# Kernel optimization log

Measured on AMD Instinct MI355X. Metric: run time of the kernel, lower is better.

The kernel has to match this reference:

```python
import jax, jax.numpy as jnp
import numpy as np

N_NODES = 100000
N_EDGES = 1600000
IN_DIM, HID_DIM, OUT_DIM = 128, 128, 64


def setup_inputs() -> dict:
    key = jax.random.key(0)
    ks = jax.random.split(key, 5)
    x = jax.random.normal(ks[0], (N_NODES, IN_DIM), dtype=jnp.float32)
    edge_index = jax.random.randint(ks[1], (2, N_EDGES), 0, N_NODES, dtype=jnp.int64)
    W1 = jax.random.normal(ks[2], (IN_DIM, HID_DIM), dtype=jnp.float32) * (1.0 / np.sqrt(IN_DIM))
    b1 = jnp.zeros((HID_DIM,), dtype=jnp.float32)
    W2 = jax.random.normal(ks[3], (HID_DIM, OUT_DIM), dtype=jnp.float32) * (1.0 / np.sqrt(HID_DIM))
    b2 = jnp.zeros((OUT_DIM,), dtype=jnp.float32)
    return {"x": x, "edge_index": edge_index, "W1": W1, "b1": b1, "W2": W2, "b2": b2}


def _gcn_conv(h, row, col, norm, b, n_nodes):
    # h: [N, F] already linearly transformed; message = norm_e * h[src]; scatter-add to dst
    msg = h[row] * norm[:, None]                      # [E+N, F]
    out = jax.ops.segment_sum(msg, col, num_segments=n_nodes)
    return out + b


def reference(x, edge_index, W1, b1, W2, b2):
    n = x.shape[0]
    loops = jnp.arange(n, dtype=edge_index.dtype)
    row = jnp.concatenate([edge_index[0], loops])     # sources (incl. self loops)
    col = jnp.concatenate([edge_index[1], loops])     # targets
    # symmetric normalization: deg over targets with unit edge weights
    deg = jax.ops.segment_sum(jnp.ones_like(col, dtype=x.dtype), col, num_segments=n)
    dinv = jnp.where(deg > 0, jax.lax.rsqrt(jnp.maximum(deg, 1.0)), 0.0)
    norm = dinv[row] * dinv[col]                      # [E+N]
    h = jax.nn.relu(_gcn_conv(x @ W1, row, col, norm, b1, n))
    out = _gcn_conv(h @ W2, row, col, norm, b2, n)
    return out.mean(axis=0)                           # [OUT_DIM]
```

## Files before the change

### kernel.cpp

```cpp
#include <hip/hip_runtime.h>

#define N_NODES 100000
#define N_EDGES 1600000
#define IN_DIM 128
#define HID_DIM 128
#define OUT_DIM 64
#define BKT_SHIFT 7
#define BKT_SIZE 128
#define NBKT ((N_NODES + BKT_SIZE - 1) / BKT_SIZE)
#define B1 256
#define HIST_N (NBKT * B1)
#define HIST_N2 (2 * HIST_N)
#define GEMM_BLKS ((N_NODES + 127) / 128)

typedef float v2f __attribute__((ext_vector_type(2)));
typedef float v4f __attribute__((ext_vector_type(4)));
typedef short v8s __attribute__((ext_vector_type(8)));

__device__ __forceinline__ int permb(int b) { return ((b & 7) << 5) | (b >> 3); }

__device__ __forceinline__ unsigned int f2bf(float f) {
  unsigned int u = __float_as_uint(f);
  return (u + 0x7FFFu + ((u >> 16) & 1u)) >> 16;
}

template <bool HI>
__device__ __forceinline__ v2f cvt8(unsigned int u) {
  return __builtin_amdgcn_cvt_pk_f32_fp8((int)u, HI);
}

__device__ __forceinline__ float wdec(unsigned int p) {
  return __uint_as_float((p >> 17) << 16);
}

__device__ __forceinline__ void load4(const void* ei, int is64, int half, int base,
                                      int* v) {
  if (is64) {
    const long long* e = (const long long*)ei + (size_t)half * N_EDGES + base;
    longlong2 a = *(const longlong2*)e;
    longlong2 b = *(const longlong2*)(e + 2);
    v[0] = (int)a.x; v[1] = (int)a.y; v[2] = (int)b.x; v[3] = (int)b.y;
  } else {
    const int* e = (const int*)ei + (size_t)half * N_EDGES + base;
    int4 a = *(const int4*)e;
    v[0] = a.x; v[1] = a.y; v[2] = a.z; v[3] = a.w;
  }
}

__device__ __forceinline__ int detect64_block(const unsigned int* ei, int* sh) {
  if (threadIdx.x == 0) *sh = 0;
  __syncthreads();
  if (ei[1 + 2 * threadIdx.x] != 0u) *sh = 1;
  __syncthreads();
  return (*sh == 0) ? 1 : 0;
}

__global__ __launch_bounds__(256) void front_kernel(const float* __restrict__ x,
                                                    const float* __restrict__ W,
                                                    const void* ei,
                                                    unsigned int* __restrict__ G,
                                                    int* hist, float* S) {
  __shared__ __align__(16) char smem[2 * 128 * 136 * 2];
  if (blockIdx.x >= GEMM_BLKS) {
    int* hd = (int*)smem;
    int* hs = hd + NBKT;
    int* sh = hs + NBKT;
    const int hb = blockIdx.x - GEMM_BLKS;
    const int pj = permb(hb);
    if (hb == 0 && threadIdx.x < HID_DIM) S[threadIdx.x] = 0.f;
    const int is64 = detect64_block((const unsigned int*)ei, sh);
    for (int k = threadIdx.x; k < NBKT; k += 256) { hd[k] = 0; hs[k] = 0; }
    __syncthreads();
    for (int g = hb * 256 + threadIdx.x; g < N_EDGES / 4; g += B1 * 256) {
      int r[4], c[4];
      load4(ei, is64, 0, g * 4, r);
      load4(ei, is64, 1, g * 4, c);
#pragma unroll
      for (int k = 0; k < 4; k++) {
        atomicAdd(&hd[c[k] >> BKT_SHIFT], 1);
        atomicAdd(&hs[r[k] >> BKT_SHIFT], 1);
      }
    }
    __syncthreads();
    for (int k = threadIdx.x; k < NBKT; k += 256) {
      hist[k * B1 + pj] = hd[k];
      hist[HIST_N + k * B1 + pj] = hs[k];
    }
    return;
  }
  typedef unsigned short us_row[136];
  us_row* lx = (us_row*)smem;
  us_row* lwt = (us_row*)(smem + 128 * 136 * 2);
  const int t = threadIdx.x;
  const int row0 = blockIdx.x * 128;

  {
    const float4* W4 = (const float4*)W;
    for (int it = 0; it < 16; ++it) {
      int idx = t + 256 * it;
      int k = idx >> 5, c4 = (idx & 31) * 4;
      float4 w = W4[idx];
      lwt[c4 + 0][k] = (unsigned short)f2bf(w.x);
      lwt[c4 + 1][k] = (unsigned short)f2bf(w.y);
      lwt[c4 + 2][k] = (unsigned short)f2bf(w.z);
      lwt[c4 + 3][k] = (unsigned short)f2bf(w.w);
    }
  }
  {
    const float4* x4 = (const float4*)(x + (size_t)row0 * IN_DIM);
    for (int it = 0; it < 16; ++it) {
      int idx = t + 256 * it;
      int r = idx >> 5, kq = (idx & 31) * 4;
      float4 v = make_float4(0.f, 0.f, 0.f, 0.f);
      if (row0 + r < N_NODES) v = x4[idx];
      unsigned int p0 = (f2bf(v.y) << 16) | f2bf(v.x);
      unsigned int p1 = (f2bf(v.w) << 16) | f2bf(v.z);
      *(uint2*)&lx[r][kq] = make_uint2(p0, p1);
    }
  }
  __syncthreads();

  const int lane = t & 63;
  const int wv = t >> 6;
  const int m0 = wv * 32;
  const int lrow = lane & 15;
  const int lk = (lane >> 4) * 8;

  v4f acc[2][8];
#pragma unroll
  for (int si = 0; si < 2; si++)
#pragma unroll
    for (int n = 0; n < 8; n++) acc[si][n] = (v4f){0.f, 0.f, 0.f, 0.f};

#pragma unroll
  for (int kk = 0; kk < 128; kk += 32) {
    v8s a0 = *(const v8s*)&lx[m0 + lrow][kk + lk];
    v8s a1 = *(const v8s*)&lx[m0 + 16 + lrow][kk + lk];
#pragma unroll
    for (int n = 0; n < 8; n++) {
      v8s b = *(const v8s*)&lwt[n * 16 + lrow][kk + lk];
      acc[0][n] = __builtin_amdgcn_mfma_f32_16x16x32_bf16(a0, b, acc[0][n], 0, 0, 0);
      acc[1][n] = __builtin_amdgcn_mfma_f32_16x16x32_bf16(a1, b, acc[1][n], 0, 0, 0);
    }
  }

  unsigned char* G8 = (unsigned char*)G;
#pragma unroll
  for (int si = 0; si < 2; si++)
#pragma unroll
    for (int n = 0; n < 8; n++) {
      int colg = n * 16 + (lane & 15);
#pragma unroll
      for (int i = 0; i < 4; i++) {
        int r = row0 + m0 + si * 16 + (lane >> 4) * 4 + i;
        if (r < N_NODES) {
          float v = acc[si][n][i];
          int pk = __builtin_amdgcn_cvt_pk_fp8_f32(v, v, 0, false);
          G8[(size_t)r * HID_DIM + colg] = (unsigned char)(pk & 0xFF);
        }
      }
    }
}

__global__ void scan1_kernel(int* arr, int* bsum, int n) {
  __shared__ int tmp[256];
  int i = blockIdx.x * 256 + threadIdx.x;
  int v = (i < n) ? arr[i] : 0;
  tmp[threadIdx.x] = v;
  __syncthreads();
  for (int off = 1; off < 256; off <<= 1) {
    int t2 = (threadIdx.x >= off) ? tmp[threadIdx.x - off] : 0;
    __syncthreads();
    tmp[threadIdx.x] += t2;
    __syncthreads();
  }
  if (i < n) arr[i] = tmp[threadIdx.x] - v;
  if (threadIdx.x == 255) bsum[blockIdx.x] = tmp[255];
}

__global__ void scan2_kernel(int* bsum, int nb) {
  __shared__ int tmp[1024];
  const int t = threadIdx.x;
  int v0 = (2 * t < nb) ? bsum[2 * t] : 0;
  int v1 = (2 * t + 1 < nb) ? bsum[2 * t + 1] : 0;
  int s = v0 + v1;
  tmp[t] = s;
  __syncthreads();
  for (int off = 1; off < 1024; off <<= 1) {
    int t2 = (t >= off) ? tmp[t - off] : 0;
    __syncthreads();
    tmp[t] += t2;
    __syncthreads();
  }
  int excl = tmp[t] - s;
  if (2 * t < nb) bsum[2 * t] = excl;
  if (2 * t + 1 < nb) bsum[2 * t + 1] = excl + v0;
}

__global__ __launch_bounds__(256) void scatter_kernel(const void* ei, const int* hist,
                                                      const int* bsum,
                                                      unsigned int* pairs) {
  __shared__ int cd[NBKT], cs[NBKT], sh[1];
  const int is64 = detect64_block((const unsigned int*)ei, sh);
  const int pj = permb(blockIdx.x);
  for (int k = threadIdx.x; k < NBKT; k += 256) {
    cd[k] = hist[k * B1 + pj] + bsum[k];
    cs[k] = hist[HIST_N + k * B1 + pj] + bsum[NBKT + k];
  }
  __syncthreads();
  for (int g = blockIdx.x * 256 + threadIdx.x; g < N_EDGES / 4; g += B1 * 256) {
    int r[4], c[4];
    load4(ei, is64, 0, g * 4, r);
    load4(ei, is64, 1, g * 4, c);
#pragma unroll
    for (int k = 0; k < 4; k++) {
      int pd = atomicAdd(&cd[c[k] >> BKT_SHIFT], 1);
      pairs[pd] = ((unsigned int)(c[k] & (BKT_SIZE - 1)) << 17) | (unsigned int)r[k];
      int ps = atomicAdd(&cs[r[k] >> BKT_SHIFT], 1);
      pairs[ps] = ((unsigned int)(r[k] & (BKT_SIZE - 1)) << 17) | (unsigned int)c[k];
    }
  }
}

__global__ __launch_bounds__(256) void csrA_kernel(const int* hist, const int* bsum,
                                                   const unsigned int* pairs,
                                                   int* rowptr, float* dinv) {
  __shared__ int cnt[BKT_SIZE], sc[BKT_SIZE];
  const int k = blockIdx.x;
  const int base = hist[k * B1] + bsum[k];
  const int end = (k == NBKT - 1) ? N_EDGES : hist[(k + 1) * B1] + bsum[k + 1];
  const int nseg = end - base;
  const int l = threadIdx.x;
  if (l < BKT_SIZE) cnt[l] = 0;
  __syncthreads();
  for (int i = l; i < nseg; i += 256) atomicAdd(&cnt[pairs[base + i] >> 17], 1);
  __syncthreads();
  if (l < BKT_SIZE) sc[l] = cnt[l];
  __syncthreads();
  for (int off = 1; off < BKT_SIZE; off <<= 1) {
    int v = (l < BKT_SIZE && l >= off) ? sc[l - off] : 0;
    __syncthreads();
    if (l < BKT_SIZE) sc[l] += v;
    __syncthreads();
  }
  if (l < BKT_SIZE) {
    int excl = sc[l] - cnt[l];
    int v = k * BKT_SIZE + l;
    if (v < N_NODES) {
      rowptr[v] = base + excl;
      dinv[v] = rsqrtf((float)(cnt[l] + 1));
    }
  }
  if (k == NBKT - 1 && l == 0) rowptr[N_NODES] = N_EDGES;
}

__global__ __launch_bounds__(256) void csrBout_kernel(const int* hist, const int* bsum,
                                                      const unsigned int* pairs,
                                                      const int* __restrict__ rowptr,
                                                      const float* __restrict__ dinv,
                                                      unsigned int* __restrict__ csr,
                                                      float* __restrict__ wacc) {
  if (blockIdx.x < NBKT) {
    __shared__ int cur[BKT_SIZE];
    const int k = blockIdx.x;
    const int base = hist[k * B1] + bsum[k];
    const int end = (k == NBKT - 1) ? N_EDGES : hist[(k + 1) * B1] + bsum[k + 1];
    const int nseg = end - base;
    const int l = threadIdx.x;
    if (l < BKT_SIZE) {
      int v = k * BKT_SIZE + l;
      cur[l] = (v < N_NODES) ? rowptr[v] : 0;
    }
    __syncthreads();
    for (int i = l; i < nseg; i += 256) {
      unsigned int pk = pairs[base + i];
      unsigned int src = pk & 0x1FFFFu;
      int pos = atomicAdd(&cur[pk >> 17], 1);
      unsigned int bits = f2bf(dinv[src]);
      csr[pos] = (bits << 17) | src;
    }
    return;
  }
  __shared__ float fb[BKT_SIZE];
  const int k = blockIdx.x - NBKT;
  const int base = hist[HIST_N + k * B1] + bsum[NBKT + k];
  const int end =
      (k == NBKT - 1) ? 2 * N_EDGES : hist[HIST_N + (k + 1) * B1] + bsum[NBKT + k + 1];
  if (threadIdx.x < BKT_SIZE) fb[threadIdx.x] = 0.f;
  __syncthreads();
  for (int i = base + threadIdx.x; i < end; i += 256) {
    unsigned int pk = pairs[i];
    atomicAdd(&fb[pk >> 17], dinv[pk & 0x1FFFFu]);
  }
  __syncthreads();
  int v = k * BKT_SIZE + threadIdx.x;
  if (threadIdx.x < BKT_SIZE && v < N_NODES) wacc[v] = fb[threadIdx.x];
}

__global__ __launch_bounds__(256) void aggregate_kernel(
    const unsigned int* __restrict__ G, const int* __restrict__ rowptr,
    const unsigned int* __restrict__ csr, const float* __restrict__ dinv,
    const float* __restrict__ wacc, const float* __restrict__ b1,
    float* __restrict__ S) {
  const int lane = threadIdx.x & 63;
  const int sub = lane & 31;
  const int half = lane >> 5;
  const int wid = blockIdx.x * 4 + (threadIdx.x >> 6);
  const int nwaves = gridDim.x * 4;
  const float4 b = ((const float4*)b1)[sub];
  v2f s01 = {0.f, 0.f}, s23 = {0.f, 0.f};

  for (int c = wid; c < N_NODES; c += nwaves) {
    const int start = rowptr[c];
    const int cnum = rowptr[c + 1] - start;
    const float d = dinv[c];
    v2f a01 = {0.f, 0.f}, a23 = {0.f, 0.f};
    if (half == 0) {
      unsigned int g = G[c * 32 + sub];
      a01 = cvt8<false>(g) * d;
      a23 = cvt8<true>(g) * d;
    }
    for (int j0 = 0; j0 < cnum; j0 += 64) {
      unsigned int pkl = 0;
      if (j0 + lane < cnum)
        pkl = __builtin_nontemporal_load(&csr[start + j0 + lane]);
      const int m = min(64, cnum - j0);
      int i = 0;
      for (; i + 8 <= m; i += 8) {
        unsigned int p0 = __shfl(pkl, i + half);
        unsigned int p1 = __shfl(pkl, i + 2 + half);
        unsigned int p2 = __shfl(pkl, i + 4 + half);
        unsigned int p3 = __shfl(pkl, i + 6 + half);
        unsigned int g0 = G[(p0 & 0x1FFFFu) * 32 + sub];
        unsigned int g1 = G[(p1 & 0x1FFFFu) * 32 + sub];
        unsigned int g2 = G[(p2 & 0x1FFFFu) * 32 + sub];
        unsigned int g3 = G[(p3 & 0x1FFFFu) * 32 + sub];
        float w0 = wdec(p0), w1 = wdec(p1), w2 = wdec(p2), w3 = wdec(p3);
        a01 += cvt8<false>(g0) * w0; a23 += cvt8<true>(g0) * w0;
        a01 += cvt8<false>(g1) * w1; a23 += cvt8<true>(g1) * w1;
        a01 += cvt8<false>(g2) * w2; a23 += cvt8<true>(g2) * w2;
        a01 += cvt8<false>(g3) * w3; a23 += cvt8<true>(g3) * w3;
      }
      for (; i + 2 <= m; i += 2) {
        unsigned int p = __shfl(pkl, i + half);
        unsigned int g = G[(p & 0x1FFFFu) * 32 + sub];
        float w = wdec(p);
        a01 += cvt8<false>(g) * w;
        a23 += cvt8<true>(g) * w;
      }
      if (i < m) {
        unsigned int p = __shfl(pkl, i);
        if (half == 0) {
          unsigned int g = G[(p & 0x1FFFFu) * 32 + sub];
          float w = wdec(p);
          a01 += cvt8<false>(g) * w;
          a23 += cvt8<true>(g) * w;
        }
      }
    }
    a01.x += __shfl(a01.x, sub + 32);
    a01.y += __shfl(a01.y, sub + 32);
    a23.x += __shfl(a23.x, sub + 32);
    a23.y += __shfl(a23.y, sub + 32);
    if (half == 0) {
      float wc = d * (wacc[c] + d);
      s01.x += wc * fmaxf(fmaf(d, a01.x, b.x), 0.f);
      s01.y += wc * fmaxf(fmaf(d, a01.y, b.y), 0.f);
      s23.x += wc * fmaxf(fmaf(d, a23.x, b.z), 0.f);
      s23.y += wc * fmaxf(fmaf(d, a23.y, b.w), 0.f);
    }
  }

  __shared__ float ls[HID_DIM];
  if (threadIdx.x < HID_DIM) ls[threadIdx.x] = 0.f;
  __syncthreads();
  if (half == 0) {
    atomicAdd(&ls[4 * sub + 0], s01.x);
    atomicAdd(&ls[4 * sub + 1], s01.y);
    atomicAdd(&ls[4 * sub + 2], s23.x);
    atomicAdd(&ls[4 * sub + 3], s23.y);
  }
  __syncthreads();
  if (threadIdx.x < HID_DIM) atomicAdd(&S[threadIdx.x], ls[threadIdx.x]);
}

__global__ void finish_kernel(const float* __restrict__ S, const float* __restrict__ W2,
                              const float* __restrict__ b2, float* __restrict__ out) {
  int j = threadIdx.x;
  float acc = 0.f;
  for (int k = 0; k < HID_DIM; k++) acc += S[k] * W2[k * OUT_DIM + j];
  out[j] = acc * (1.0f / N_NODES) + b2[j];
}

extern "C" void kernel_launch(void* const* d_in, const int* in_sizes, int n_in,
                              void* d_out, int out_size, void* d_ws, size_t ws_size,
                              hipStream_t stream) {
  const float* x  = (const float*)d_in[0];
  const void*  ei = d_in[1];
  const float* W1 = (const float*)d_in[2];
  const float* b1 = (const float*)d_in[3];
  const float* W2 = (const float*)d_in[4];
  const float* b2 = (const float*)d_in[5];
  float* out = (float*)d_out;

  char* p = (char*)d_ws;
  size_t off = 0;
  auto alloc = [&](size_t bytes) -> void* {
    void* r = p + off;
    off = (off + bytes + 63) & ~(size_t)63;
    return r;
  };
  int*   hist   = (int*)alloc((size_t)HIST_N2 * 4);
  int*   bsum   = (int*)alloc(2048 * 4);
  unsigned int* pairs = (unsigned int*)alloc((size_t)2 * N_EDGES * 4);
  int*   rowptr = (int*)alloc(((size_t)N_NODES + 1) * 4);
  unsigned int* csr = (unsigned int*)alloc((size_t)N_EDGES * 4);
  float* dinv   = (float*)alloc((size_t)N_NODES * 4);
  float* wacc   = (float*)alloc((size_t)N_NODES * 4);
  float* S      = (float*)alloc(HID_DIM * 4);
  unsigned int* G = (unsigned int*)alloc((size_t)N_NODES * HID_DIM);
  (void)ws_size; (void)n_in; (void)in_sizes; (void)out_size;

  const int NBH = HIST_N2 / 256;

  front_kernel<<<GEMM_BLKS + B1, 256, 0, stream>>>(x, W1, ei, G, hist, S);
  scan1_kernel<<<NBH, 256, 0, stream>>>(hist, bsum, HIST_N2);
  scan2_kernel<<<1, 1024, 0, stream>>>(bsum, NBH);
  scatter_kernel<<<B1, 256, 0, stream>>>(ei, hist, bsum, pairs);
  csrA_kernel<<<NBKT, 256, 0, stream>>>(hist, bsum, pairs, rowptr, dinv);
  csrBout_kernel<<<2 * NBKT, 256, 0, stream>>>(hist, bsum, pairs, rowptr, dinv, csr,
                                               wacc);
  aggregate_kernel<<<2048, 256, 0, stream>>>(G, rowptr, csr, dinv, wacc, b1, S);
  finish_kernel<<<1, 64, 0, stream>>>(S, W2, b2, out);
}
```

Measured before the change: 272.7 us.

## Restructure aggregation: quarter-wave edges, contiguous node chunks, prefetched CSR

The aggregation kernel now splits each wave into four 16-lane groups. Each lane gathers 8 bytes (uint2) of the fp8 feature row, so a wave processes four edges per gather step instead of two. Each wave takes a contiguous chunk of 13 nodes, loads their rowptr, dinv and wacc values once into lanes, and prefetches the next node's CSR entries while the current node is being processed. The changes aim to raise memory-level parallelism and cut per-node scalar loads. The cost is more register pressure, a two-step xor-shuffle reduction per node, and a masked tail path. Grid size with NPW=13 gives 8192 waves covering 106496 nodes, so all nodes are covered.

```diff
diff --git a/kernel.cpp b/kernel.cpp
--- a/kernel.cpp
+++ b/kernel.cpp
@@ -12,6 +12,8 @@
 #define HIST_N (NBKT * B1)
 #define HIST_N2 (2 * HIST_N)
 #define GEMM_BLKS ((N_NODES + 127) / 128)
+#define AGG_BLKS 2048
+#define NPW 13
 
 typedef float v2f __attribute__((ext_vector_type(2)));
 typedef float v4f __attribute__((ext_vector_type(4)));
@@ -31,6 +33,12 @@
 
 __device__ __forceinline__ float wdec(unsigned int p) {
   return __uint_as_float((p >> 17) << 16);
+}
+
+__device__ __forceinline__ float redq(float v) {
+  v += __shfl_xor(v, 16);
+  v += __shfl_xor(v, 32);
+  return v;
 }
 
 __device__ __forceinline__ void load4(const void* ei, int is64, int half, int base,
@@ -303,82 +311,122 @@
     const float* __restrict__ wacc, const float* __restrict__ b1,
     float* __restrict__ S) {
   const int lane = threadIdx.x & 63;
-  const int sub = lane & 31;
-  const int half = lane >> 5;
+  const int q = lane >> 4;
+  const int r = lane & 15;
   const int wid = blockIdx.x * 4 + (threadIdx.x >> 6);
-  const int nwaves = gridDim.x * 4;
-  const float4 b = ((const float4*)b1)[sub];
-  v2f s01 = {0.f, 0.f}, s23 = {0.f, 0.f};
-
-  for (int c = wid; c < N_NODES; c += nwaves) {
-    const int start = rowptr[c];
-    const int cnum = rowptr[c + 1] - start;
-    const float d = dinv[c];
-    v2f a01 = {0.f, 0.f}, a23 = {0.f, 0.f};
-    if (half == 0) {
-      unsigned int g = G[c * 32 + sub];
-      a01 = cvt8<false>(g) * d;
-      a23 = cvt8<true>(g) * d;
-    }
+  const int c0 = wid * NPW;
+  const uint2* __restrict__ G2 = (const uint2*)G;
+
+  int rp = 0;
+  float dvv = 0.f, wvv = 0.f;
+  {
+    const int ci = c0 + lane;
+    if (lane <= NPW && ci <= N_NODES) rp = rowptr[ci];
+    if (lane < NPW && ci < N_NODES) { dvv = dinv[ci]; wvv = wacc[ci]; }
+  }
+  const float4 bA = ((const float4*)b1)[2 * r];
+  const float4 bB = ((const float4*)b1)[2 * r + 1];
+
+  v2f s01 = {0.f, 0.f}, s23 = {0.f, 0.f}, s45 = {0.f, 0.f}, s67 = {0.f, 0.f};
+
+  const int nn = (c0 < N_NODES) ? min(NPW, N_NODES - c0) : 0;
+
+  int sNxt = __shfl(rp, 0);
+  int eNxt = __shfl(rp, 1);
+  unsigned int pwNxt = 0;
+  if (nn > 0 && sNxt + lane < eNxt)
+    pwNxt = __builtin_nontemporal_load(&csr[sNxt + lane]);
+
+  for (int k = 0; k < nn; ++k) {
+    const int sc = sNxt;
+    const int cnum = eNxt - sNxt;
+    unsigned int pw = pwNxt;
+    const float d = __shfl(dvv, k);
+    const float wa = __shfl(wvv, k);
+    if (k + 1 < nn) {
+      sNxt = __shfl(rp, k + 1);
+      eNxt = __shfl(rp, k + 2);
+      pwNxt = 0;
+      if (sNxt + lane < eNxt)
+        pwNxt = __builtin_nontemporal_load(&csr[sNxt + lane]);
+    }
+
+    v2f a01 = {0.f, 0.f}, a23 = {0.f, 0.f}, a45 = {0.f, 0.f}, a67 = {0.f, 0.f};
+    if (q == 0) {
+      uint2 g = G2[(size_t)(c0 + k) * 16 + r];
+      a01 += cvt8<false>(g.x) * d; a23 += cvt8<true>(g.x) * d;
+      a45 += cvt8<false>(g.y) * d; a67 += cvt8<true>(g.y) * d;
+    }
+
     for (int j0 = 0; j0 < cnum; j0 += 64) {
-      unsigned int pkl = 0;
-      if (j0 + lane < cnum)
-        pkl = __builtin_nontemporal_load(&csr[start + j0 + lane]);
+      if (j0 > 0) {
+        pw = 0;
+        if (j0 + lane < cnum)
+          pw = __builtin_nontemporal_load(&csr[sc + j0 + lane]);
+      }
       const int m = min(64, cnum - j0);
       int i = 0;
-      for (; i + 8 <= m; i += 8) {
-        unsigned int p0 = __shfl(pkl, i + half);
-        unsigned int p1 = __shfl(pkl, i + 2 + half);
-        unsigned int p2 = __shfl(pkl, i + 4 + half);
-        unsigned int p3 = __shfl(pkl, i + 6 + half);
-        unsigned int g0 = G[(p0 & 0x1FFFFu) * 32 + sub];
-        unsigned int g1 = G[(p1 & 0x1FFFFu) * 32 + sub];
-        unsigned int g2 = G[(p2 & 0x1FFFFu) * 32 + sub];
-        unsigned int g3 = G[(p3 & 0x1FFFFu) * 32 + sub];
-        float w0 = wdec(p0), w1 = wdec(p1), w2 = wdec(p2), w3 = wdec(p3);
-        a01 += cvt8<false>(g0) * w0; a23 += cvt8<true>(g0) * w0;
-        a01 += cvt8<false>(g1) * w1; a23 += cvt8<true>(g1) * w1;
-        a01 += cvt8<false>(g2) * w2; a23 += cvt8<true>(g2) * w2;
-        a01 += cvt8<false>(g3) * w3; a23 += cvt8<true>(g3) * w3;
-      }
-      for (; i + 2 <= m; i += 2) {
-        unsigned int p = __shfl(pkl, i + half);
-        unsigned int g = G[(p & 0x1FFFFu) * 32 + sub];
-        float w = wdec(p);
-        a01 += cvt8<false>(g) * w;
-        a23 += cvt8<true>(g) * w;
+      for (; i + 16 <= m; i += 16) {
+        float w[4];
+        uint2 g[4];
+#pragma unroll
+        for (int t = 0; t < 4; ++t) {
+          unsigned int p = __shfl(pw, i + 4 * t + q);
+          w[t] = wdec(p);
+          g[t] = G2[(size_t)(p & 0x1FFFFu) * 16 + r];
+        }
+#pragma unroll
+        for (int t = 0; t < 4; ++t) {
+          a01 += cvt8<false>(g[t].x) * w[t]; a23 += cvt8<true>(g[t].x) * w[t];
+          a45 += cvt8<false>(g[t].y) * w[t]; a67 += cvt8<true>(g[t].y) * w[t];
+        }
       }
       if (i < m) {
-        unsigned int p = __shfl(pkl, i);
-        if (half == 0) {
-          unsigned int g = G[(p & 0x1FFFFu) * 32 + sub];
-          float w = wdec(p);
-          a01 += cvt8<false>(g) * w;
-          a23 += cvt8<true>(g) * w;
+        float w[4];
+        uint2 g[4];
+#pragma unroll
+        for (int t = 0; t < 4; ++t) {
+          const int e = i + 4 * t + q;
+          unsigned int p = __shfl(pw, e & 63);
+          const bool vld = e < m;
+          w[t] = vld ? wdec(p) : 0.f;
+          g[t] = make_uint2(0u, 0u);
+          if (vld) g[t] = G2[(size_t)(p & 0x1FFFFu) * 16 + r];
+        }
+#pragma unroll
+        for (int t = 0; t < 4; ++t) {
+          a01 += cvt8<false>(g[t].x) * w[t]; a23 += cvt8<true>(g[t].x) * w[t];
+          a45 += cvt8<false>(g[t].y) * w[t]; a67 += cvt8<true>(g[t].y) * w[t];
         }
       }
     }
-    a01.x += __shfl(a01.x, sub + 32);
-    a01.y += __shfl(a01.y, sub + 32);
-    a23.x += __shfl(a23.x, sub + 32);
-    a23.y += __shfl(a23.y, sub + 32);
-    if (half == 0) {
-      float wc = d * (wacc[c] + d);
-      s01.x += wc * fmaxf(fmaf(d, a01.x, b.x), 0.f);
-      s01.y += wc * fmaxf(fmaf(d, a01.y, b.y), 0.f);
-      s23.x += wc * fmaxf(fmaf(d, a23.x, b.z), 0.f);
-      s23.y += wc * fmaxf(fmaf(d, a23.y, b.w), 0.f);
+
+    a01.x = redq(a01.x); a01.y = redq(a01.y);
+    a23.x = redq(a23.x); a23.y = redq(a23.y);
+    a45.x = redq(a45.x); a45.y = redq(a45.y);
+    a67.x = redq(a67.x); a67.y = redq(a67.y);
+
+    if (q == 0) {
+      const float wc = d * (wa + d);
+      s01.x += wc * fmaxf(fmaf(d, a01.x, bA.x), 0.f);
+      s01.y += wc * fmaxf(fmaf(d, a01.y, bA.y), 0.f);
+      s23.x += wc * fmaxf(fmaf(d, a23.x, bA.z), 0.f);
+      s23.y += wc * fmaxf(fmaf(d, a23.y, bA.w), 0.f);
+      s45.x += wc * fmaxf(fmaf(d, a45.x, bB.x), 0.f);
+      s45.y += wc * fmaxf(fmaf(d, a45.y, bB.y), 0.f);
+      s67.x += wc * fmaxf(fmaf(d, a67.x, bB.z), 0.f);
+      s67.y += wc * fmaxf(fmaf(d, a67.y, bB.w), 0.f);
     }
   }
 
   __shared__ float ls[HID_DIM];
   if (threadIdx.x < HID_DIM) ls[threadIdx.x] = 0.f;
   __syncthreads();
-  if (half == 0) {
-    atomicAdd(&ls[4 * sub + 0], s01.x);
-    atomicAdd(&ls[4 * sub + 1], s01.y);
-    atomicAdd(&ls[4 * sub + 2], s23.x);
-    atomicAdd(&ls[4 * sub + 3], s23.y);
+  if (q == 0) {
+    atomicAdd(&ls[8 * r + 0], s01.x); atomicAdd(&ls[8 * r + 1], s01.y);
+    atomicAdd(&ls[8 * r + 2], s23.x); atomicAdd(&ls[8 * r + 3], s23.y);
+    atomicAdd(&ls[8 * r + 4], s45.x); atomicAdd(&ls[8 * r + 5], s45.y);
+    atomicAdd(&ls[8 * r + 6], s67.x); atomicAdd(&ls[8 * r + 7], s67.y);
   }
   __syncthreads();
   if (threadIdx.x < HID_DIM) atomicAdd(&S[threadIdx.x], ls[threadIdx.x]);
@@ -430,6 +478,6 @@
   csrA_kernel<<<NBKT, 256, 0, stream>>>(hist, bsum, pairs, rowptr, dinv);
   csrBout_kernel<<<2 * NBKT, 256, 0, stream>>>(hist, bsum, pairs, rowptr, dinv, csr,
                                                wacc);
-  aggregate_kernel<<<2048, 256, 0, stream>>>(G, rowptr, csr, dinv, wacc, b1, S);
+  aggregate_kernel<<<AGG_BLKS, 256, 0, stream>>>(G, rowptr, csr, dinv, wacc, b1, S);
   finish_kernel<<<1, 64, 0, stream>>>(S, W2, b2, out);
 }
```

Result: no change. 270.4 us (-0.8%).
